# Kernel tuning notes

Measured on AMD Instinct MI355X. Metric: run time of the kernel, lower is better.

The kernel has to match this reference:

```python
import jax, jax.numpy as jnp
import numpy as np

D_MODEL = 2048
N_HEADS = 16
D_HEAD = D_MODEL // N_HEADS


def setup_inputs() -> dict:
    key = jax.random.key(0)
    kx, kq, kk, kv, ko = jax.random.split(key, 5)
    s = 1.0 / np.sqrt(D_MODEL)
    return {
        "x": jax.random.normal(kx, (4, 2048, D_MODEL), dtype=jnp.float32),
        "Wq": jax.random.normal(kq, (D_MODEL, D_MODEL), dtype=jnp.float32) * s,
        "Wk": jax.random.normal(kk, (D_MODEL, D_MODEL), dtype=jnp.float32) * s,
        "Wv": jax.random.normal(kv, (D_MODEL, D_MODEL), dtype=jnp.float32) * s,
        "Wo": jax.random.normal(ko, (D_MODEL, D_MODEL), dtype=jnp.float32) * s,
    }


def reference(x, Wq, Wk, Wv, Wo):
    B, S, _ = x.shape
    scale = D_HEAD ** (-0.5)
    # project and split heads: [B, H, S, Dh]
    def split_heads(t):
        return t.reshape(B, S, N_HEADS, D_HEAD).transpose(0, 2, 1, 3)
    q = split_heads(x @ Wq.T)
    k = split_heads(x @ Wk.T)
    v = split_heads(x @ Wv.T)
    sim = jnp.einsum("bhsd,bhtd->bhst", q, k) * scale  # [B,H,S,S]
    causal = jnp.tril(jnp.ones((S, S), dtype=bool))
    sim = jnp.where(causal[None, None], sim, -jnp.inf)
    weights = jax.nn.softmax(sim, axis=-1)
    out = jnp.einsum("bhst,bhtd->bhsd", weights, v)
    out = out.transpose(0, 2, 1, 3).reshape(B, S, D_MODEL)
    return out @ Wo.T
```

## Files before the change

### kernel.cpp

```cpp
#include <hip/hip_runtime.h>

typedef float f32x4 __attribute__((ext_vector_type(4)));
typedef _Float16 f16x8 __attribute__((ext_vector_type(8)));
typedef _Float16 f16x4 __attribute__((ext_vector_type(4)));
typedef unsigned int u32;

#define GLDS16(g, l)                                                        \
  __builtin_amdgcn_global_load_lds(                                         \
      (const __attribute__((address_space(1))) u32*)(g),                    \
      (__attribute__((address_space(3))) u32*)(l), 16, 0, 0)

__global__ void cast_all(const float* __restrict__ x, const float* __restrict__ wq,
                         const float* __restrict__ wk, const float* __restrict__ wv,
                         const float* __restrict__ wo, _Float16* __restrict__ xb,
                         _Float16* __restrict__ wqb, _Float16* __restrict__ wkb,
                         _Float16* __restrict__ wvb, _Float16* __restrict__ wob) {
  const int stride = gridDim.x * blockDim.x;
  const int NX = 4194304;
  const int NW = 1048576;
  for (int i = blockIdx.x * blockDim.x + threadIdx.x; i < NX + 4 * NW; i += stride) {
    const float* src;
    _Float16* dst;
    int off;
    if (i < NX) {
      src = x; dst = xb; off = i;
    } else {
      const int j = i - NX;
      const int s = j >> 20;
      off = j & (NW - 1);
      src = (s == 0) ? wq : (s == 1) ? wk : (s == 2) ? wv : wo;
      dst = (s == 0) ? wqb : (s == 1) ? wkb : (s == 2) ? wvb : wob;
    }
    float4 f = ((const float4*)src)[off];
    f16x4 h = {(_Float16)f.x, (_Float16)f.y, (_Float16)f.z, (_Float16)f.w};
    ((f16x4*)dst)[off] = h;
  }
}

template <int MODE>
__global__ __launch_bounds__(512, 2) void gemm256(
    const _Float16* __restrict__ A, const _Float16* __restrict__ B,
    void* __restrict__ Cout, int M, int N, int K) {
  __shared__ _Float16 SA[2][16384];
  __shared__ _Float16 SB[2][16384];
  const int tid = threadIdx.x;
  const int lane = tid & 63, w = tid >> 6;
  const int l15 = lane & 15, g = lane >> 4;
  const int wm = w >> 2, wn = w & 3;
  const int nbn = N >> 8;
  const int nwg = gridDim.x;
  int bid = blockIdx.x;
  bid = (bid & 7) * (nwg >> 3) + (bid >> 3);
  const int tm = bid / nbn, tn = bid % nbn;

  const _Float16* Ab = A + (size_t)tm * 256 * K;
  const _Float16* Bb = B + (size_t)tn * 256 * K;
  const int rr = tid >> 3;
  const int cx = (lane & 7) ^ (lane >> 3);
  const size_t goff = (size_t)rr * K + cx * 8;
  const int ldst = w * 512;
  const int swz = l15 & 7;

  auto STG_A = [&](int buf, int ha, int rd, int kt) {
    GLDS16(Ab + (size_t)(ha * 128 + rd * 64) * K + kt + goff,
           &SA[buf][ha * 8192 + rd * 4096 + ldst]);
  };
  auto STG_B = [&](int buf, int hb, int rd, int kt) {
    GLDS16(Bb + (size_t)(hb * 128 + rd * 64) * K + kt + goff,
           &SB[buf][hb * 8192 + rd * 4096 + ldst]);
  };

  f32x4 acc[8][4] = {};
  f16x8 a[4][2], b0[2][2], b1[2][2];

  auto LDA = [&](int buf, int mh) {
#pragma unroll
    for (int ml = 0; ml < 4; ++ml)
#pragma unroll
      for (int kk = 0; kk < 2; ++kk)
        a[ml][kk] = *(const f16x8*)(&SA[buf][wm * 8192 + mh * 4096 +
                                             (ml * 16 + l15) * 64 +
                                             ((kk * 4 + g) ^ swz) * 8]);
  };
  auto LDB = [&](int buf, int nh, f16x8 (*bb)[2]) {
#pragma unroll
    for (int nl = 0; nl < 2; ++nl)
#pragma unroll
      for (int kk = 0; kk < 2; ++kk)
        bb[nl][kk] = *(const f16x8*)(&SB[buf][(wn >> 1) * 8192 + (wn & 1) * 4096 +
                                              (nh * 32 + nl * 16 + l15) * 64 +
                                              ((kk * 4 + g) ^ swz) * 8]);
  };
  auto MM = [&](int mh, int nh, f16x8 (*bb)[2]) {
    __builtin_amdgcn_s_setprio(1);
#pragma unroll
    for (int ml = 0; ml < 4; ++ml)
#pragma unroll
      for (int nl = 0; nl < 2; ++nl)
#pragma unroll
        for (int kk = 0; kk < 2; ++kk)
          acc[mh * 4 + ml][nh * 2 + nl] = __builtin_amdgcn_mfma_f32_16x16x32_f16(
              a[ml][kk], bb[nl][kk], acc[mh * 4 + ml][nh * 2 + nl], 0, 0, 0);
    __builtin_amdgcn_s_setprio(0);
  };

  STG_A(0, 0, 0, 0); STG_A(0, 1, 0, 0);
  STG_A(0, 0, 1, 0); STG_A(0, 1, 1, 0);
  STG_B(0, 0, 0, 0); STG_B(0, 0, 1, 0);
  STG_B(0, 1, 0, 0); STG_B(0, 1, 1, 0);
  STG_A(1, 0, 0, 64); STG_A(1, 1, 0, 64);

  const int nit = K >> 7;
  for (int it = 0; it < nit; ++it) {
    const bool lastI = (it == nit - 1);
    const int kq = it * 128 + 64;
    const int kp = it * 128 + 128;
    const int kq2 = it * 128 + 192;
    STG_B(1, 0, 0, kq); STG_B(1, 0, 1, kq);
    asm volatile("s_waitcnt vmcnt(4)\ns_barrier" ::: "memory");
    LDA(0, 0); LDB(0, 0, b0);
    MM(0, 0, b0);
    STG_B(1, 1, 0, kq); STG_B(1, 1, 1, kq);
    asm volatile("s_barrier" ::: "memory");
    LDB(0, 1, b1);
    MM(0, 1, b1);
    STG_A(1, 0, 1, kq); STG_A(1, 1, 1, kq);
    asm volatile("s_barrier" ::: "memory");
    LDA(0, 1);
    MM(1, 0, b0);
    if (!lastI) { STG_A(0, 0, 0, kp); STG_A(0, 1, 0, kp); }
    asm volatile("s_barrier" ::: "memory");
    MM(1, 1, b1);
    if (!lastI) {
      STG_A(0, 0, 1, kp); STG_A(0, 1, 1, kp);
      asm volatile("s_waitcnt vmcnt(6)\ns_barrier" ::: "memory");
    } else {
      asm volatile("s_waitcnt vmcnt(2)\ns_barrier" ::: "memory");
    }
    LDA(1, 0); LDB(1, 0, b0);
    MM(0, 0, b0);
    if (!lastI) { STG_B(0, 0, 0, kp); STG_B(0, 0, 1, kp); }
    asm volatile("s_barrier" ::: "memory");
    LDB(1, 1, b1);
    MM(0, 1, b1);
    if (!lastI) {
      STG_B(0, 1, 0, kp); STG_B(0, 1, 1, kp);
      asm volatile("s_waitcnt vmcnt(8)\ns_barrier" ::: "memory");
    } else {
      asm volatile("s_waitcnt vmcnt(0)\ns_barrier" ::: "memory");
    }
    LDA(1, 1);
    MM(1, 0, b0);
    if (!lastI) { STG_A(1, 0, 0, kq2); STG_A(1, 1, 0, kq2); }
    asm volatile("s_barrier" ::: "memory");
    MM(1, 1, b1);
    asm volatile("s_barrier" ::: "memory");
  }

  const float QSCL = 0.12751654f;
#pragma unroll
  for (int mi = 0; mi < 8; ++mi) {
#pragma unroll
    for (int ni = 0; ni < 4; ++ni) {
      const int m0 = tm * 256 + wm * 128 + mi * 16 + g * 4;
      const int n = tn * 256 + wn * 64 + ni * 16 + l15;
      if (MODE == 0) {
        _Float16* C = (_Float16*)Cout;
#pragma unroll
        for (int j = 0; j < 4; ++j)
          C[(size_t)(m0 + j) * N + n] = (_Float16)acc[mi][ni][j];
      } else if (MODE == 4) {
        _Float16* C = (_Float16*)Cout;
#pragma unroll
        for (int j = 0; j < 4; ++j)
          C[(size_t)(m0 + j) * N + n] = (_Float16)(acc[mi][ni][j] * QSCL);
      } else if (MODE == 1) {
        float* C = (float*)Cout;
#pragma unroll
        for (int j = 0; j < 4; ++j)
          C[(size_t)(m0 + j) * N + n] = acc[mi][ni][j];
      } else {
        _Float16* C = (_Float16*)Cout;
        const int bb2 = m0 >> 11, t0 = m0 & 2047;
        const int hh = n >> 7, d = n & 127;
        f16x4 v = {(_Float16)acc[mi][ni][0], (_Float16)acc[mi][ni][1],
                   (_Float16)acc[mi][ni][2], (_Float16)acc[mi][ni][3]};
        *(f16x4*)(C + (size_t)((bb2 * 16 + hh) * 128 + d) * 2048 + t0) = v;
      }
    }
  }
}

__global__ __launch_bounds__(512, 4) void attn_fwd(
    const _Float16* __restrict__ Q, const _Float16* __restrict__ Km,
    const _Float16* __restrict__ VT, _Float16* __restrict__ Aout) {
  __shared__ _Float16 Kl[2][8192];
  __shared__ _Float16 Vl[2][8192];
  __shared__ _Float16 Pl[8][1024];
  const int tid = threadIdx.x;
  const int lane = tid & 63, w = tid >> 6;
  const int l15 = lane & 15, g = lane >> 4;
  const int bid = blockIdx.x;
  const int head = bid & 63;
  const int qt = 15 - (bid >> 6);
  const int b = head >> 4, h = head & 15;
  const int qbase = qt * 128;
  const float MBIAS = 8.6561699f;
  const int nkv = 2 * (qt + 1);

  f16x8 qf[4];
  {
    const _Float16* qp =
        Q + (size_t)(b * 2048 + qbase + w * 16 + l15) * 2048 + h * 128 + g * 8;
#pragma unroll
    for (int kk = 0; kk < 4; ++kk) qf[kk] = *(const f16x8*)(qp + kk * 32);
  }
  f16x8 ones;
#pragma unroll
  for (int i = 0; i < 8; ++i) ones[i] = (_Float16)1.0f;
  f32x4 o[8];
  f32x4 o_sum = {0.f, 0.f, 0.f, 0.f};
  {
    f32x4 z = {0.f, 0.f, 0.f, 0.f};
#pragma unroll
    for (int dt = 0; dt < 8; ++dt) o[dt] = z;
  }

  const int s3 = l15 & 7;
  int kfb[4], pwb[4];
#pragma unroll
  for (int kk = 0; kk < 4; ++kk) kfb[kk] = l15 * 128 + 8 * ((kk * 4 + g) ^ l15);
  const int vfb0 = l15 * 64 + 8 * (g ^ s3);
  const int vfb1 = l15 * 64 + 8 * ((4 + g) ^ s3);
  const int g1 = g >> 1, ge4 = (g & 1) * 4;
#pragma unroll
  for (int kt = 0; kt < 4; ++kt)
    pwb[kt] = l15 * 64 + ((kt * 2 + g1) ^ s3) * 8 + ge4;
  const int afo0 = l15 * 64 + (g ^ s3) * 8;
  const int afo1 = l15 * 64 + ((4 + g) ^ s3) * 8;

  const _Float16 *gK0, *gK1, *gV0, *gV1;
  {
    const int c0 = w * 64 + lane, c1 = (w + 8) * 64 + lane;
    const int tt0 = c0 >> 4, dc0 = (c0 & 15) ^ (tt0 & 15);
    const int tt1 = c1 >> 4, dc1 = (c1 & 15) ^ (tt1 & 15);
    gK0 = Km + (size_t)(b * 2048 + tt0) * 2048 + h * 128 + dc0 * 8;
    gK1 = Km + (size_t)(b * 2048 + tt1) * 2048 + h * 128 + dc1 * 8;
    const int d0 = c0 >> 3, tc0 = (c0 & 7) ^ (d0 & 7);
    const int d1 = c1 >> 3, tc1 = (c1 & 7) ^ (d1 & 7);
    gV0 = VT + (size_t)((b * 16 + h) * 128 + d0) * 2048 + tc0 * 8;
    gV1 = VT + (size_t)((b * 16 + h) * 128 + d1) * 2048 + tc1 * 8;
  }
  GLDS16(gK0, &Kl[0][w * 512]);
  GLDS16(gK1, &Kl[0][(w + 8) * 512]);
  GLDS16(gV0, &Vl[0][w * 512]);
  GLDS16(gV1, &Vl[0][(w + 8) * 512]);

#define ATTN_TILE(T, CUR, MASKED, LASTT)                                      \
  {                                                                           \
    __syncthreads();                                                          \
    if ((T) + 1 < nkv) {                                                      \
      GLDS16(gK0 + (size_t)((T) + 1) * 131072, &Kl[(CUR) ^ 1][w * 512]);      \
      GLDS16(gK1 + (size_t)((T) + 1) * 131072, &Kl[(CUR) ^ 1][(w + 8) * 512]);\
      GLDS16(gV0 + (size_t)((T) + 1) * 64, &Vl[(CUR) ^ 1][w * 512]);          \
      GLDS16(gV1 + (size_t)((T) + 1) * 64, &Vl[(CUR) ^ 1][(w + 8) * 512]);    \
    }                                                                         \
    if (!(LASTT) || w >= 4) {                                                 \
      float s[4][4];                                                          \
      __builtin_amdgcn_s_setprio(1);                                          \
      _Pragma("unroll") for (int kt = 0; kt < 4; ++kt) {                      \
        f32x4 acc = {-MBIAS, -MBIAS, -MBIAS, -MBIAS};                         \
        _Pragma("unroll") for (int kk = 0; kk < 4; ++kk) {                    \
          f16x8 kf = *(const f16x8*)(&Kl[CUR][kfb[kk] + kt * 2048]);          \
          acc = __builtin_amdgcn_mfma_f32_16x16x32_f16(kf, qf[kk], acc, 0, 0, 0);\
        }                                                                     \
        _Pragma("unroll") for (int j = 0; j < 4; ++j) s[kt][j] = acc[j];      \
      }                                                                       \
      __builtin_amdgcn_s_setprio(0);                                          \
      if (MASKED) {                                                           \
        const int query = qbase + w * 16 + l15;                               \
        const int kvb = (T) * 64;                                             \
        _Pragma("unroll") for (int kt = 0; kt < 4; ++kt)                      \
          _Pragma("unroll") for (int j = 0; j < 4; ++j)                       \
            if (kvb + kt * 16 + g * 4 + j > query) s[kt][j] = -1e30f;         \
      }                                                                       \
      _Pragma("unroll") for (int kt = 0; kt < 4; ++kt) {                      \
        auto lo = __builtin_amdgcn_cvt_pkrtz(exp2f(s[kt][0]), exp2f(s[kt][1]));\
        auto hi = __builtin_amdgcn_cvt_pkrtz(exp2f(s[kt][2]), exp2f(s[kt][3]));\
        f16x4 pv = {(_Float16)lo[0], (_Float16)lo[1],                         \
                    (_Float16)hi[0], (_Float16)hi[1]};                        \
        *(f16x4*)(&Pl[w][pwb[kt]]) = pv;                                      \
      }                                                                       \
      f16x8 af0 = *(const f16x8*)(&Pl[w][afo0]);                              \
      f16x8 af1 = *(const f16x8*)(&Pl[w][afo1]);                              \
      __builtin_amdgcn_s_setprio(1);                                          \
      o_sum = __builtin_amdgcn_mfma_f32_16x16x32_f16(af0, ones, o_sum, 0, 0, 0);\
      o_sum = __builtin_amdgcn_mfma_f32_16x16x32_f16(af1, ones, o_sum, 0, 0, 0);\
      _Pragma("unroll") for (int dt = 0; dt < 8; ++dt) {                      \
        f16x8 vf0 = *(const f16x8*)(&Vl[CUR][vfb0 + dt * 1024]);              \
        o[dt] = __builtin_amdgcn_mfma_f32_16x16x32_f16(af0, vf0, o[dt], 0, 0, 0);\
        f16x8 vf1 = *(const f16x8*)(&Vl[CUR][vfb1 + dt * 1024]);              \
        o[dt] = __builtin_amdgcn_mfma_f32_16x16x32_f16(af1, vf1, o[dt], 0, 0, 0);\
      }                                                                       \
      __builtin_amdgcn_s_setprio(0);                                          \
    }                                                                         \
  }

  int t = 0;
  for (; t + 3 < nkv; t += 2) {
    ATTN_TILE(t, 0, false, false);
    ATTN_TILE(t + 1, 1, false, false);
  }
  ATTN_TILE(t, 0, true, false);
  ATTN_TILE(t + 1, 1, true, true);
#undef ATTN_TILE

  float inv[4];
#pragma unroll
  for (int j = 0; j < 4; ++j) inv[j] = 1.0f / o_sum[j];
  const size_t obase =
      (size_t)(b * 2048 + qbase + w * 16 + g * 4) * 2048 + h * 128 + l15;
#pragma unroll
  for (int dt = 0; dt < 8; ++dt)
#pragma unroll
    for (int j = 0; j < 4; ++j)
      Aout[obase + (size_t)j * 2048 + dt * 16] = (_Float16)(o[dt][j] * inv[j]);
}

extern "C" void kernel_launch(void* const* d_in, const int* in_sizes, int n_in,
                              void* d_out, int out_size, void* d_ws, size_t ws_size,
                              hipStream_t stream) {
  const float* x = (const float*)d_in[0];
  const float* Wq = (const float*)d_in[1];
  const float* Wk = (const float*)d_in[2];
  const float* Wv = (const float*)d_in[3];
  const float* Wo = (const float*)d_in[4];
  float* out = (float*)d_out;
  char* ws = (char*)d_ws;

  const size_t SZ_X = 33554432;
  const size_t SZ_W = 8388608;
  _Float16* xb = (_Float16*)(ws);
  _Float16* Wqb = (_Float16*)(ws + SZ_X);
  _Float16* Wkb = (_Float16*)(ws + SZ_X + SZ_W);
  _Float16* Wvb = (_Float16*)(ws + SZ_X + 2 * SZ_W);
  _Float16* Wob = (_Float16*)(ws + SZ_X + 3 * SZ_W);
  _Float16* Qb = (_Float16*)(ws + SZ_X + 4 * SZ_W);
  _Float16* Kb = (_Float16*)(ws + 2 * SZ_X + 4 * SZ_W);
  _Float16* VTb = (_Float16*)(ws + 3 * SZ_X + 4 * SZ_W);
  _Float16* AOb = (_Float16*)(ws + 4 * SZ_X + 4 * SZ_W);

  cast_all<<<4096, 256, 0, stream>>>(x, Wq, Wk, Wv, Wo, xb, Wqb, Wkb, Wvb, Wob);

  const int M = 8192, N = 2048, K = 2048;
  const int grid = (M / 256) * (N / 256);
  gemm256<4><<<grid, 512, 0, stream>>>(xb, Wqb, Qb, M, N, K);
  gemm256<0><<<grid, 512, 0, stream>>>(xb, Wkb, Kb, M, N, K);
  gemm256<2><<<grid, 512, 0, stream>>>(xb, Wvb, VTb, M, N, K);

  attn_fwd<<<1024, 512, 0, stream>>>(Qb, Kb, VTb, AOb);

  gemm256<1><<<grid, 512, 0, stream>>>(AOb, Wob, out, M, N, K);
}
```

Before: 391.4 us.

## Double-buffer A fragments and prefetch LDS reads ahead of MFMA in GEMM loop

Restructures the GEMM main loop so LDS-to-register loads for the next sub-tile are issued right after the current MFMA block. A fragments now alternate between two register sets, and the first fragment loads are hoisted before the loop. Global-to-LDS staging is reordered and the waitcnt thresholds are changed. The goal is to hide LDS read latency behind matrix-core work, at the cost of more VGPRs, which could lower occupancy or cause spills.

```diff
diff --git a/kernel.cpp b/kernel.cpp
--- a/kernel.cpp
+++ b/kernel.cpp
@@ -71,27 +71,27 @@
   };
 
   f32x4 acc[8][4] = {};
-  f16x8 a[4][2], b0[2][2], b1[2][2];
-
-  auto LDA = [&](int buf, int mh) {
+  f16x8 aE[4][2], aO[4][2], b0[2][2], b1[2][2];
+
+  auto LDA = [&](int buf, int rd, f16x8 (*dst)[2]) {
 #pragma unroll
     for (int ml = 0; ml < 4; ++ml)
 #pragma unroll
       for (int kk = 0; kk < 2; ++kk)
-        a[ml][kk] = *(const f16x8*)(&SA[buf][wm * 8192 + mh * 4096 +
-                                             (ml * 16 + l15) * 64 +
-                                             ((kk * 4 + g) ^ swz) * 8]);
-  };
-  auto LDB = [&](int buf, int nh, f16x8 (*bb)[2]) {
+        dst[ml][kk] = *(const f16x8*)(&SA[buf][wm * 8192 + rd * 4096 +
+                                               (ml * 16 + l15) * 64 +
+                                               ((kk * 4 + g) ^ swz) * 8]);
+  };
+  auto LDB = [&](int buf, int nh, f16x8 (*dst)[2]) {
 #pragma unroll
     for (int nl = 0; nl < 2; ++nl)
 #pragma unroll
       for (int kk = 0; kk < 2; ++kk)
-        bb[nl][kk] = *(const f16x8*)(&SB[buf][(wn >> 1) * 8192 + (wn & 1) * 4096 +
-                                              (nh * 32 + nl * 16 + l15) * 64 +
-                                              ((kk * 4 + g) ^ swz) * 8]);
-  };
-  auto MM = [&](int mh, int nh, f16x8 (*bb)[2]) {
+        dst[nl][kk] = *(const f16x8*)(&SB[buf][(wn >> 1) * 8192 + (wn & 1) * 4096 +
+                                               (nh * 32 + nl * 16 + l15) * 64 +
+                                               ((kk * 4 + g) ^ swz) * 8]);
+  };
+  auto MM = [&](int mh, int nh, f16x8 (*aa)[2], f16x8 (*bb)[2]) {
     __builtin_amdgcn_s_setprio(1);
 #pragma unroll
     for (int ml = 0; ml < 4; ++ml)
@@ -100,61 +100,63 @@
 #pragma unroll
         for (int kk = 0; kk < 2; ++kk)
           acc[mh * 4 + ml][nh * 2 + nl] = __builtin_amdgcn_mfma_f32_16x16x32_f16(
-              a[ml][kk], bb[nl][kk], acc[mh * 4 + ml][nh * 2 + nl], 0, 0, 0);
+              aa[ml][kk], bb[nl][kk], acc[mh * 4 + ml][nh * 2 + nl], 0, 0, 0);
     __builtin_amdgcn_s_setprio(0);
   };
 
   STG_A(0, 0, 0, 0); STG_A(0, 1, 0, 0);
-  STG_A(0, 0, 1, 0); STG_A(0, 1, 1, 0);
   STG_B(0, 0, 0, 0); STG_B(0, 0, 1, 0);
   STG_B(0, 1, 0, 0); STG_B(0, 1, 1, 0);
+  STG_A(0, 0, 1, 0); STG_A(0, 1, 1, 0);
   STG_A(1, 0, 0, 64); STG_A(1, 1, 0, 64);
+  STG_B(1, 0, 0, 64); STG_B(1, 0, 1, 64);
+  asm volatile("s_waitcnt vmcnt(4)\ns_barrier" ::: "memory");
+  LDA(0, 0, aE); LDB(0, 0, b0);
 
   const int nit = K >> 7;
   for (int it = 0; it < nit; ++it) {
     const bool lastI = (it == nit - 1);
-    const int kq = it * 128 + 64;
-    const int kp = it * 128 + 128;
-    const int kq2 = it * 128 + 192;
-    STG_B(1, 0, 0, kq); STG_B(1, 0, 1, kq);
-    asm volatile("s_waitcnt vmcnt(4)\ns_barrier" ::: "memory");
-    LDA(0, 0); LDB(0, 0, b0);
-    MM(0, 0, b0);
-    STG_B(1, 1, 0, kq); STG_B(1, 1, 1, kq);
-    asm volatile("s_barrier" ::: "memory");
+    const int kQ = it * 128 + 64;
+    const int kP = it * 128 + 128;
+    const int kQ2 = it * 128 + 192;
+    STG_B(1, 1, 0, kQ); STG_B(1, 1, 1, kQ);
+    asm volatile("s_barrier" ::: "memory");
+    MM(0, 0, aE, b0);
     LDB(0, 1, b1);
-    MM(0, 1, b1);
-    STG_A(1, 0, 1, kq); STG_A(1, 1, 1, kq);
-    asm volatile("s_barrier" ::: "memory");
-    LDA(0, 1);
-    MM(1, 0, b0);
-    if (!lastI) { STG_A(0, 0, 0, kp); STG_A(0, 1, 0, kp); }
-    asm volatile("s_barrier" ::: "memory");
-    MM(1, 1, b1);
+    STG_A(1, 0, 1, kQ); STG_A(1, 1, 1, kQ);
+    asm volatile("s_barrier" ::: "memory");
+    MM(0, 1, aE, b1);
+    LDA(0, 1, aO);
+    if (!lastI) { STG_A(0, 0, 0, kP); STG_A(0, 1, 0, kP); }
+    asm volatile("s_barrier" ::: "memory");
+    MM(1, 0, aO, b0);
     if (!lastI) {
-      STG_A(0, 0, 1, kp); STG_A(0, 1, 1, kp);
-      asm volatile("s_waitcnt vmcnt(6)\ns_barrier" ::: "memory");
-    } else {
-      asm volatile("s_waitcnt vmcnt(2)\ns_barrier" ::: "memory");
-    }
-    LDA(1, 0); LDB(1, 0, b0);
-    MM(0, 0, b0);
-    if (!lastI) { STG_B(0, 0, 0, kp); STG_B(0, 0, 1, kp); }
-    asm volatile("s_barrier" ::: "memory");
-    LDB(1, 1, b1);
-    MM(0, 1, b1);
-    if (!lastI) {
-      STG_B(0, 1, 0, kp); STG_B(0, 1, 1, kp);
-      asm volatile("s_waitcnt vmcnt(8)\ns_barrier" ::: "memory");
+      STG_B(0, 0, 0, kP); STG_B(0, 0, 1, kP);
+      asm volatile("s_waitcnt vmcnt(4)\ns_barrier" ::: "memory");
     } else {
       asm volatile("s_waitcnt vmcnt(0)\ns_barrier" ::: "memory");
     }
-    LDA(1, 1);
-    MM(1, 0, b0);
-    if (!lastI) { STG_A(1, 0, 0, kq2); STG_A(1, 1, 0, kq2); }
-    asm volatile("s_barrier" ::: "memory");
-    MM(1, 1, b1);
-    asm volatile("s_barrier" ::: "memory");
+    MM(1, 1, aO, b1);
+    LDA(1, 0, aE); LDB(1, 0, b0);
+    if (!lastI) { STG_B(0, 1, 0, kP); STG_B(0, 1, 1, kP); }
+    asm volatile("s_barrier" ::: "memory");
+    MM(0, 0, aE, b0);
+    LDB(1, 1, b1);
+    if (!lastI) { STG_A(0, 0, 1, kP); STG_A(0, 1, 1, kP); }
+    asm volatile("s_barrier" ::: "memory");
+    MM(0, 1, aE, b1);
+    LDA(1, 1, aO);
+    if (!lastI) { STG_A(1, 0, 0, kQ2); STG_A(1, 1, 0, kQ2); }
+    asm volatile("s_barrier" ::: "memory");
+    MM(1, 0, aO, b0);
+    if (!lastI) {
+      STG_B(1, 0, 0, kQ2); STG_B(1, 0, 1, kQ2);
+      asm volatile("s_waitcnt vmcnt(4)\ns_barrier" ::: "memory");
+    } else {
+      asm volatile("s_waitcnt vmcnt(0)\ns_barrier" ::: "memory");
+    }
+    MM(1, 1, aO, b1);
+    LDA(0, 0, aE); LDB(0, 0, b0);
   }
 
   const float QSCL = 0.12751654f;
```

Measured after the change: 381.2 us. -2.6%, faster.
